# Optimization experiments

Hardware: AMD Instinct MI355X
Metric: run time of the kernel (lower is better)

The kernel has to match this reference:

```python
import jax, jax.numpy as jnp
import numpy as np

N_NODES = 100000
N_EDGES = 1600000
IN_CH = 128
HID = 64
OUT_CH = 10
N_GRAPHS = 64
NEG_SLOPE = 0.2   # GATv2Conv default negative_slope
EPS = 1e-16       # PyG softmax eps


def setup_inputs() -> dict:
    key = jax.random.key(0)
    ks = jax.random.split(key, 10)
    x = jax.random.normal(ks[0], (N_NODES, IN_CH), dtype=jnp.float32)
    edge_index = jax.random.randint(ks[1], (2, N_EDGES), 0, N_NODES, dtype=jnp.int64)
    batch = jnp.sort(jax.random.randint(ks[2], (N_NODES,), 0, N_GRAPHS, dtype=jnp.int64))
    s = 1.0 / np.sqrt(IN_CH)
    Wl = jax.random.uniform(ks[3], (IN_CH, HID), jnp.float32, -s, s)   # lin_l (source)
    Wr = jax.random.uniform(ks[4], (IN_CH, HID), jnp.float32, -s, s)   # lin_r (target)
    att = jax.random.uniform(ks[5], (HID,), jnp.float32, -1.0 / np.sqrt(HID), 1.0 / np.sqrt(HID))
    bias = jnp.zeros((HID,), jnp.float32)
    sf = 1.0 / np.sqrt(HID)
    fc_w = jax.random.uniform(ks[6], (HID, OUT_CH), jnp.float32, -sf, sf)
    fc_b = jax.random.uniform(ks[7], (OUT_CH,), jnp.float32, -sf, sf)
    return {"x": x, "Wl": Wl, "Wr": Wr, "att": att, "bias": bias,
            "fc_w": fc_w, "fc_b": fc_b, "edge_index": edge_index, "batch": batch}


def reference(x, Wl, Wr, att, bias, fc_w, fc_b, edge_index, batch):
    src, tgt = edge_index[0], edge_index[1]
    # GATv2Conv, heads=1: separate linear for source/target
    xl = x @ Wl                         # [N, H] messages (source side)
    xr = x @ Wr                         # [N, H] target side
    z = xl[src] + xr[tgt]               # [E, H]
    e = jnp.where(z > 0, z, NEG_SLOPE * z) @ att   # [E]
    # segment softmax over incoming edges of each target node
    m = jax.ops.segment_max(e, tgt, num_segments=N_NODES)      # [N]
    a = jnp.exp(e - m[tgt])                                    # [E]
    denom = jax.ops.segment_sum(a, tgt, num_segments=N_NODES)  # [N]
    alpha = a / (denom[tgt] + EPS)                             # [E]
    out = jax.ops.segment_sum(alpha[:, None] * xl[src], tgt, num_segments=N_NODES)
    out = out + bias                                           # [N, H]
    # global mean pool over graphs
    cnt = jax.ops.segment_sum(jnp.ones((N_NODES,), out.dtype), batch, num_segments=N_GRAPHS)
    pooled = jax.ops.segment_sum(out, batch, num_segments=N_GRAPHS) / jnp.maximum(cnt, 1.0)[:, None]
    h = jnp.where(pooled > 0, pooled, 0.01 * pooled)           # F.leaky_relu default slope
    # dropout is identity in eval / p=0
    return h @ fc_w + fc_b                                     # [G, OUT_CH]
```

## Files before the change

### kernel.cpp

```cpp
#include <hip/hip_runtime.h>
#include <hip/hip_bf16.h>

#define NN 100000
#define EE 1600000
#define CIN 128
#define HID 64
#define NG 64
#define NOUT 10
#define BSZ 32
#define NB 3125
#define CAP 768

__global__ __launch_bounds__(256) void k_gemm(
    const float* __restrict__ x, const float* __restrict__ Wl,
    const float* __restrict__ Wr, float* __restrict__ xl,
    float* __restrict__ xr) {
  __shared__ float Wlds[64 * 128];
  __shared__ float Xlds[64 * 68];
  const int tid = threadIdx.x;
  const int cg = tid & 31;
  const int ng = tid >> 5;
  const int ntiles = (NN + 63) >> 6;

  for (int tile = blockIdx.x; tile < ntiles; tile += gridDim.x) {
    const int nb = tile << 6;
    float acc[8][4];
#pragma unroll
    for (int i = 0; i < 8; ++i)
#pragma unroll
      for (int j = 0; j < 4; ++j) acc[i][j] = 0.f;

    for (int kc = 0; kc < CIN; kc += 64) {
      __syncthreads();
#pragma unroll
      for (int it = 0; it < 4; ++it) {
        int f = tid * 4 + it * 1024;
        int kk = f >> 6, c = f & 63;
        *(float4*)(Wlds + kk * 128 + c) =
            *(const float4*)(Wl + (kc + kk) * HID + c);
        *(float4*)(Wlds + kk * 128 + 64 + c) =
            *(const float4*)(Wr + (kc + kk) * HID + c);
      }
#pragma unroll
      for (int it = 0; it < 4; ++it) {
        int f = tid * 4 + it * 1024;
        int n = f >> 6, k = f & 63;
        int node = nb + n;
        float4 v;
        if (node < NN)
          v = *(const float4*)(x + (long)node * CIN + kc + k);
        else
          v = make_float4(0.f, 0.f, 0.f, 0.f);
        *(float4*)(Xlds + n * 68 + k) = v;
      }
      __syncthreads();

#pragma unroll 4
      for (int kk = 0; kk < 64; ++kk) {
        float4 w = *(const float4*)(Wlds + kk * 128 + cg * 4);
#pragma unroll
        for (int i = 0; i < 8; ++i) {
          float xv = Xlds[(ng * 8 + i) * 68 + kk];
          acc[i][0] = fmaf(xv, w.x, acc[i][0]);
          acc[i][1] = fmaf(xv, w.y, acc[i][1]);
          acc[i][2] = fmaf(xv, w.z, acc[i][2]);
          acc[i][3] = fmaf(xv, w.w, acc[i][3]);
        }
      }
    }
    const int cbase = cg * 4;
    float* dst = (cbase < 64) ? xl : xr;
    const int cb = cbase & 63;
#pragma unroll
    for (int i = 0; i < 8; ++i) {
      int node = nb + ng * 8 + i;
      if (node < NN) {
        float4 v = make_float4(acc[i][0], acc[i][1], acc[i][2], acc[i][3]);
        *(float4*)(dst + (long)node * HID + cb) = v;
      }
    }
  }
}

__global__ __launch_bounds__(256) void k_bucket(const int* __restrict__ ei,
                                                int* __restrict__ gcur,
                                                unsigned int* __restrict__ buckets) {
  __shared__ int hist[NB];
  __shared__ int lbase[NB];
  const int tid = threadIdx.x;
  const int base = blockIdx.x * 4096;
  for (int b = tid; b < NB; b += 256) hist[b] = 0;
  __syncthreads();
#pragma unroll
  for (int i = 0; i < 16; ++i) {
    int j = base + i * 256 + tid;
    if (j < EE) {
      int t = ei[EE + j];
      atomicAdd(&hist[t >> 5], 1);
    }
  }
  __syncthreads();
  for (int b = tid; b < NB; b += 256) {
    int c = hist[b];
    lbase[b] = (c > 0) ? atomicAdd(&gcur[b], c) : 0;
    hist[b] = 0;
  }
  __syncthreads();
#pragma unroll
  for (int i = 0; i < 16; ++i) {
    int j = base + i * 256 + tid;
    if (j < EE) {
      int s = ei[j];
      int t = ei[EE + j];
      int b2 = t >> 5;
      int lp = atomicAdd(&hist[b2], 1);
      int p = lbase[b2] + lp;
      if (p < CAP)
        buckets[(long)b2 * CAP + p] = ((unsigned)s << 5) | (unsigned)(t & 31);
    }
  }
}

__global__ __launch_bounds__(256) void k_pull2(
    const int* __restrict__ gcnt, const unsigned int* __restrict__ buckets,
    const float* __restrict__ xl, const float* __restrict__ xr,
    const float* __restrict__ att, const float* __restrict__ bias,
    const int* __restrict__ batch, float* __restrict__ pooled,
    float* __restrict__ cnt) {
  __shared__ unsigned int staged[CAP];
  __shared__ int lds_src[CAP];
  __shared__ int hist[BSZ];
  __shared__ int starts[BSZ + 1], cur[BSZ];
  __shared__ float pool2[2][HID];
  __shared__ float cnt2[2];
  const int tid = threadIdx.x;
  const int b = blockIdx.x;
  const int t0 = b << 5;
  const int ecnt = min(gcnt[b], CAP);

  if (tid < BSZ) hist[tid] = 0;
  if (tid < 2 * HID) ((float*)pool2)[tid] = 0.f;
  if (tid < 2) cnt2[tid] = 0.f;
  __syncthreads();

  for (int i = tid; i < ecnt; i += 256) {
    unsigned v = buckets[(long)b * CAP + i];
    staged[i] = v;
    atomicAdd(&hist[v & 31u], 1);
  }
  __syncthreads();

  if (tid < BSZ) {
    int v = hist[tid];
    int sum = v;
#pragma unroll
    for (int off = 1; off < BSZ; off <<= 1) {
      int t = __shfl_up(sum, off, 64);
      if (tid >= off) sum += t;
    }
    starts[tid] = sum - v;
    cur[tid] = sum - v;
    if (tid == BSZ - 1) starts[BSZ] = sum;
  }
  __syncthreads();

  for (int i = tid; i < ecnt; i += 256) {
    unsigned v = staged[i];
    int d = v & 31u;
    int p = atomicAdd(&cur[d], 1);
    lds_src[p] = (int)(v >> 5);
  }
  __syncthreads();

  const int g = tid & 15;
  const int grp = tid >> 4;
  const float4 a4 = *(const float4*)(att + g * 4);
  const float4 b4 = *(const float4*)(bias + g * 4);
  const int g0 = batch[t0];

#pragma unroll
  for (int rep = 0; rep < 2; ++rep) {
    const int d = grp * 2 + rep;
    const int n = t0 + d;
    const float4 xt = *(const float4*)(xr + (long)n * HID + g * 4);
    float4 acc = make_float4(0.f, 0.f, 0.f, 0.f);
    float den = 0.f;
    const int e0 = starts[d], e1 = starts[d + 1];
    int e = e0;
    for (; e + 1 < e1; e += 2) {
      const int s0 = lds_src[e];
      const int s1 = lds_src[e + 1];
      const float4 xs0 = *(const float4*)(xl + (long)s0 * HID + g * 4);
      const float4 xs1 = *(const float4*)(xl + (long)s1 * HID + g * 4);
      float zx0 = xs0.x + xt.x, zy0 = xs0.y + xt.y;
      float zz0 = xs0.z + xt.z, zw0 = xs0.w + xt.w;
      float zx1 = xs1.x + xt.x, zy1 = xs1.y + xt.y;
      float zz1 = xs1.z + xt.z, zw1 = xs1.w + xt.w;
      zx0 = zx0 > 0.f ? zx0 : 0.2f * zx0;
      zy0 = zy0 > 0.f ? zy0 : 0.2f * zy0;
      zz0 = zz0 > 0.f ? zz0 : 0.2f * zz0;
      zw0 = zw0 > 0.f ? zw0 : 0.2f * zw0;
      zx1 = zx1 > 0.f ? zx1 : 0.2f * zx1;
      zy1 = zy1 > 0.f ? zy1 : 0.2f * zy1;
      zz1 = zz1 > 0.f ? zz1 : 0.2f * zz1;
      zw1 = zw1 > 0.f ? zw1 : 0.2f * zw1;
      float p0 = zx0 * a4.x + zy0 * a4.y + zz0 * a4.z + zw0 * a4.w;
      float p1 = zx1 * a4.x + zy1 * a4.y + zz1 * a4.z + zw1 * a4.w;
      p0 += __shfl_xor(p0, 1, 16);
      p1 += __shfl_xor(p1, 1, 16);
      p0 += __shfl_xor(p0, 2, 16);
      p1 += __shfl_xor(p1, 2, 16);
      p0 += __shfl_xor(p0, 4, 16);
      p1 += __shfl_xor(p1, 4, 16);
      p0 += __shfl_xor(p0, 8, 16);
      p1 += __shfl_xor(p1, 8, 16);
      const float a0 = __expf(p0);
      const float a1 = __expf(p1);
      den += a0 + a1;
      acc.x = fmaf(a0, xs0.x, acc.x);
      acc.y = fmaf(a0, xs0.y, acc.y);
      acc.z = fmaf(a0, xs0.z, acc.z);
      acc.w = fmaf(a0, xs0.w, acc.w);
      acc.x = fmaf(a1, xs1.x, acc.x);
      acc.y = fmaf(a1, xs1.y, acc.y);
      acc.z = fmaf(a1, xs1.z, acc.z);
      acc.w = fmaf(a1, xs1.w, acc.w);
    }
    if (e < e1) {
      const int s0 = lds_src[e];
      const float4 xs0 = *(const float4*)(xl + (long)s0 * HID + g * 4);
      float zx0 = xs0.x + xt.x, zy0 = xs0.y + xt.y;
      float zz0 = xs0.z + xt.z, zw0 = xs0.w + xt.w;
      zx0 = zx0 > 0.f ? zx0 : 0.2f * zx0;
      zy0 = zy0 > 0.f ? zy0 : 0.2f * zy0;
      zz0 = zz0 > 0.f ? zz0 : 0.2f * zz0;
      zw0 = zw0 > 0.f ? zw0 : 0.2f * zw0;
      float p0 = zx0 * a4.x + zy0 * a4.y + zz0 * a4.z + zw0 * a4.w;
      p0 += __shfl_xor(p0, 1, 16);
      p0 += __shfl_xor(p0, 2, 16);
      p0 += __shfl_xor(p0, 4, 16);
      p0 += __shfl_xor(p0, 8, 16);
      const float a0 = __expf(p0);
      den += a0;
      acc.x = fmaf(a0, xs0.x, acc.x);
      acc.y = fmaf(a0, xs0.y, acc.y);
      acc.z = fmaf(a0, xs0.z, acc.z);
      acc.w = fmaf(a0, xs0.w, acc.w);
    }
    const float inv = 1.f / (den + 1e-16f);
    float4 v4 = make_float4(fmaf(acc.x, inv, b4.x), fmaf(acc.y, inv, b4.y),
                            fmaf(acc.z, inv, b4.z), fmaf(acc.w, inv, b4.w));
    const int gr = batch[n];
    const int idx = gr - g0;
    if (idx >= 0 && idx < 2) {
      atomicAdd(&pool2[idx][g * 4 + 0], v4.x);
      atomicAdd(&pool2[idx][g * 4 + 1], v4.y);
      atomicAdd(&pool2[idx][g * 4 + 2], v4.z);
      atomicAdd(&pool2[idx][g * 4 + 3], v4.w);
      if (g == 0) atomicAdd(&cnt2[idx], 1.f);
    } else {
      atomicAdd(pooled + gr * HID + g * 4 + 0, v4.x);
      atomicAdd(pooled + gr * HID + g * 4 + 1, v4.y);
      atomicAdd(pooled + gr * HID + g * 4 + 2, v4.z);
      atomicAdd(pooled + gr * HID + g * 4 + 3, v4.w);
      if (g == 0) atomicAdd(cnt + gr, 1.f);
    }
  }
  __syncthreads();
  if (tid < 2 * HID) {
    const int which = tid >> 6, c = tid & 63;
    const int gg = g0 + which;
    const float val = pool2[which][c];
    if (gg < NG && val != 0.f) atomicAdd(pooled + gg * HID + c, val);
  }
  if (tid < 2) {
    const int gg = g0 + tid;
    if (gg < NG && cnt2[tid] != 0.f) atomicAdd(cnt + gg, cnt2[tid]);
  }
}

__global__ void k_final(const float* __restrict__ pooled,
                        const float* __restrict__ cnt,
                        const float* __restrict__ fc_w,
                        const float* __restrict__ fc_b,
                        float* __restrict__ out) {
  const int tid = threadIdx.x;
  if (tid >= NG * NOUT) return;
  const int gr = tid / NOUT, o = tid % NOUT;
  const float cg = fmaxf(cnt[gr], 1.0f);
  float acc = fc_b[o];
#pragma unroll 8
  for (int h = 0; h < HID; ++h) {
    float pv = pooled[gr * HID + h] / cg;
    float hv = pv > 0.f ? pv : 0.01f * pv;
    acc = fmaf(hv, fc_w[h * NOUT + o], acc);
  }
  out[gr * NOUT + o] = acc;
}

extern "C" void kernel_launch(void* const* d_in, const int* in_sizes, int n_in,
                              void* d_out, int out_size, void* d_ws,
                              size_t ws_size, hipStream_t stream) {
  const float* x = (const float*)d_in[0];
  const float* Wl = (const float*)d_in[1];
  const float* Wr = (const float*)d_in[2];
  const float* att = (const float*)d_in[3];
  const float* bias = (const float*)d_in[4];
  const float* fc_w = (const float*)d_in[5];
  const float* fc_b = (const float*)d_in[6];
  const int* ei = (const int*)d_in[7];
  const int* batch = (const int*)d_in[8];
  float* out = (float*)d_out;

  float* ws = (float*)d_ws;
  float* xl = ws;
  float* xr = xl + (long)NN * HID;
  unsigned int* buckets = (unsigned int*)(xr + (long)NN * HID);
  int* gcur = (int*)(buckets + (long)NB * CAP);
  float* pooled = (float*)(gcur + NB);
  float* cnt = pooled + NG * HID;

  hipMemsetAsync(gcur, 0, (size_t)(NB + NG * HID + NG) * sizeof(int), stream);

  k_gemm<<<768, 256, 0, stream>>>(x, Wl, Wr, xl, xr);
  k_bucket<<<(EE + 4095) / 4096, 256, 0, stream>>>(ei, gcur, buckets);
  k_pull2<<<NB, 256, 0, stream>>>(gcur, buckets, xl, xr, att, bias, batch,
                                  pooled, cnt);
  k_final<<<1, NG * NOUT, 0, stream>>>(pooled, cnt, fc_w, fc_b, out);
}
```

Before: 284.1 us.

## Use bf16 MFMA GEMM, store xl/xr as bf16, simplify edge bucketing

The projection GEMM now runs on bf16 MFMA instructions, using swizzled LDS tiles and a small kernel that pre-transposes and converts the weights. Its outputs xl/xr are stored as bf16, which halves the bytes of every random gather in the edge-pull kernel. The bucketing kernel drops its per-block LDS histogram and instead does one global atomic per edge. The bf16 rounding of x, W and the projections adds numerical error, and the per-edge global atomics may contend more than the old two-pass scheme.

Result: slower. 354.5 us (+24.8%).

```diff
diff --git a/kernel.cpp b/kernel.cpp
--- a/kernel.cpp
+++ b/kernel.cpp
@@ -11,119 +11,138 @@
 #define NB 3125
 #define CAP 768
 
+typedef short s16x8 __attribute__((ext_vector_type(8)));
+typedef float f32x4 __attribute__((ext_vector_type(4)));
+
+__device__ __forceinline__ unsigned short f2b(float f) {
+  unsigned int b = __float_as_uint(f);
+  return (unsigned short)((b + 0x7FFFu + ((b >> 16) & 1u)) >> 16);
+}
+__device__ __forceinline__ float b2f(unsigned short h) {
+  return __uint_as_float(((unsigned int)h) << 16);
+}
+
+__global__ __launch_bounds__(256) void k_prep(const float* __restrict__ Wl,
+                                              const float* __restrict__ Wr,
+                                              unsigned short* __restrict__ Wt) {
+  int flat = blockIdx.x * 2048 + threadIdx.x;
+  for (int i = 0; i < 8; ++i, flat += 256) {
+    int n = flat & 127, k = flat >> 7;
+    float v = (n < 64) ? Wl[k * 64 + n] : Wr[k * 64 + (n - 64)];
+    Wt[n * 128 + k] = f2b(v);
+  }
+}
+
 __global__ __launch_bounds__(256) void k_gemm(
-    const float* __restrict__ x, const float* __restrict__ Wl,
-    const float* __restrict__ Wr, float* __restrict__ xl,
-    float* __restrict__ xr) {
-  __shared__ float Wlds[64 * 128];
-  __shared__ float Xlds[64 * 68];
+    const float* __restrict__ x, const unsigned short* __restrict__ Wt,
+    unsigned short* __restrict__ xl, unsigned short* __restrict__ xr) {
+  __shared__ unsigned short A[128 * 128];
+  __shared__ unsigned short B[128 * 128];
   const int tid = threadIdx.x;
-  const int cg = tid & 31;
-  const int ng = tid >> 5;
-  const int ntiles = (NN + 63) >> 6;
-
-  for (int tile = blockIdx.x; tile < ntiles; tile += gridDim.x) {
-    const int nb = tile << 6;
-    float acc[8][4];
-#pragma unroll
-    for (int i = 0; i < 8; ++i)
-#pragma unroll
-      for (int j = 0; j < 4; ++j) acc[i][j] = 0.f;
-
-    for (int kc = 0; kc < CIN; kc += 64) {
-      __syncthreads();
-#pragma unroll
-      for (int it = 0; it < 4; ++it) {
-        int f = tid * 4 + it * 1024;
-        int kk = f >> 6, c = f & 63;
-        *(float4*)(Wlds + kk * 128 + c) =
-            *(const float4*)(Wl + (kc + kk) * HID + c);
-        *(float4*)(Wlds + kk * 128 + 64 + c) =
-            *(const float4*)(Wr + (kc + kk) * HID + c);
+  const int lane = tid & 63;
+  const int w = tid >> 6;
+  const int nb = blockIdx.x * 128;
+
+  {
+    int u = tid;
+#pragma unroll
+    for (int i = 0; i < 8; ++i, u += 256) {
+      int n = u >> 4, slot = u & 15;
+      uint4 v = *(const uint4*)((const char*)Wt + u * 16);
+      int addr = n * 256 + ((slot * 16) ^ ((n & 7) << 4));
+      *(uint4*)((char*)B + addr) = v;
+    }
+  }
+  {
+    int f = tid;
+#pragma unroll
+    for (int i = 0; i < 16; ++i, f += 256) {
+      int row = f >> 5, c4 = f & 31;
+      int node = nb + row;
+      float4 v = make_float4(0.f, 0.f, 0.f, 0.f);
+      if (node < NN) v = *(const float4*)(x + (long)node * CIN + c4 * 4);
+      uint2 p;
+      p.x = (unsigned)f2b(v.x) | ((unsigned)f2b(v.y) << 16);
+      p.y = (unsigned)f2b(v.z) | ((unsigned)f2b(v.w) << 16);
+      int base16 = row * 256 + (((c4 >> 1) << 4) ^ ((row & 7) << 4));
+      *(uint2*)((char*)A + base16 + (c4 & 1) * 8) = p;
+    }
+  }
+  __syncthreads();
+
+  const int m0 = w * 32;
+  f32x4 acc[2][8];
+#pragma unroll
+  for (int mt = 0; mt < 2; ++mt)
+#pragma unroll
+    for (int nt = 0; nt < 8; ++nt) acc[mt][nt] = (f32x4){0.f, 0.f, 0.f, 0.f};
+
+#pragma unroll
+  for (int ks = 0; ks < 4; ++ks) {
+    const int kb2 = (ks * 32 + (lane >> 4) * 8) * 2;
+    const int r0 = m0 + (lane & 15);
+    const int r1 = r0 + 16;
+    s16x8 a0 = *(const s16x8*)((char*)A + r0 * 256 + (kb2 ^ ((r0 & 7) << 4)));
+    s16x8 a1 = *(const s16x8*)((char*)A + r1 * 256 + (kb2 ^ ((r1 & 7) << 4)));
+#pragma unroll
+    for (int nt = 0; nt < 8; ++nt) {
+      const int col = nt * 16 + (lane & 15);
+      s16x8 b =
+          *(const s16x8*)((char*)B + col * 256 + (kb2 ^ ((col & 7) << 4)));
+      acc[0][nt] =
+          __builtin_amdgcn_mfma_f32_16x16x32_bf16(a0, b, acc[0][nt], 0, 0, 0);
+      acc[1][nt] =
+          __builtin_amdgcn_mfma_f32_16x16x32_bf16(a1, b, acc[1][nt], 0, 0, 0);
+    }
+  }
+  __syncthreads();
+
+#pragma unroll
+  for (int mt = 0; mt < 2; ++mt) {
+    const int rowb = m0 + mt * 16 + (lane >> 4) * 4;
+#pragma unroll
+    for (int nt = 0; nt < 8; ++nt) {
+      const int col = nt * 16 + (lane & 15);
+#pragma unroll
+      for (int r = 0; r < 4; ++r)
+        *((unsigned short*)A + (rowb + r) * 128 + col) = f2b(acc[mt][nt][r]);
+    }
+  }
+  __syncthreads();
+
+  {
+    int u = tid;
+#pragma unroll
+    for (int i = 0; i < 8; ++i, u += 256) {
+      int row = u >> 4, slot = u & 15;
+      int node = nb + row;
+      if (node < NN) {
+        uint4 v = *(const uint4*)((const char*)A + row * 256 + slot * 16);
+        if (slot < 8)
+          *(uint4*)((char*)xl + (long)node * 128 + slot * 16) = v;
+        else
+          *(uint4*)((char*)xr + (long)node * 128 + (slot - 8) * 16) = v;
       }
-#pragma unroll
-      for (int it = 0; it < 4; ++it) {
-        int f = tid * 4 + it * 1024;
-        int n = f >> 6, k = f & 63;
-        int node = nb + n;
-        float4 v;
-        if (node < NN)
-          v = *(const float4*)(x + (long)node * CIN + kc + k);
-        else
-          v = make_float4(0.f, 0.f, 0.f, 0.f);
-        *(float4*)(Xlds + n * 68 + k) = v;
-      }
-      __syncthreads();
-
-#pragma unroll 4
-      for (int kk = 0; kk < 64; ++kk) {
-        float4 w = *(const float4*)(Wlds + kk * 128 + cg * 4);
-#pragma unroll
-        for (int i = 0; i < 8; ++i) {
-          float xv = Xlds[(ng * 8 + i) * 68 + kk];
-          acc[i][0] = fmaf(xv, w.x, acc[i][0]);
-          acc[i][1] = fmaf(xv, w.y, acc[i][1]);
-          acc[i][2] = fmaf(xv, w.z, acc[i][2]);
-          acc[i][3] = fmaf(xv, w.w, acc[i][3]);
-        }
-      }
-    }
-    const int cbase = cg * 4;
-    float* dst = (cbase < 64) ? xl : xr;
-    const int cb = cbase & 63;
-#pragma unroll
-    for (int i = 0; i < 8; ++i) {
-      int node = nb + ng * 8 + i;
-      if (node < NN) {
-        float4 v = make_float4(acc[i][0], acc[i][1], acc[i][2], acc[i][3]);
-        *(float4*)(dst + (long)node * HID + cb) = v;
-      }
-    }
-  }
-}
-
-__global__ __launch_bounds__(256) void k_bucket(const int* __restrict__ ei,
-                                                int* __restrict__ gcur,
-                                                unsigned int* __restrict__ buckets) {
-  __shared__ int hist[NB];
-  __shared__ int lbase[NB];
-  const int tid = threadIdx.x;
-  const int base = blockIdx.x * 4096;
-  for (int b = tid; b < NB; b += 256) hist[b] = 0;
-  __syncthreads();
-#pragma unroll
-  for (int i = 0; i < 16; ++i) {
-    int j = base + i * 256 + tid;
-    if (j < EE) {
-      int t = ei[EE + j];
-      atomicAdd(&hist[t >> 5], 1);
-    }
-  }
-  __syncthreads();
-  for (int b = tid; b < NB; b += 256) {
-    int c = hist[b];
-    lbase[b] = (c > 0) ? atomicAdd(&gcur[b], c) : 0;
-    hist[b] = 0;
-  }
-  __syncthreads();
-#pragma unroll
-  for (int i = 0; i < 16; ++i) {
-    int j = base + i * 256 + tid;
-    if (j < EE) {
-      int s = ei[j];
-      int t = ei[EE + j];
-      int b2 = t >> 5;
-      int lp = atomicAdd(&hist[b2], 1);
-      int p = lbase[b2] + lp;
-      if (p < CAP)
-        buckets[(long)b2 * CAP + p] = ((unsigned)s << 5) | (unsigned)(t & 31);
-    }
-  }
+    }
+  }
+}
+
+__global__ __launch_bounds__(256) void k_bucket(
+    const int* __restrict__ ei, int* __restrict__ gcur,
+    unsigned int* __restrict__ buckets) {
+  const int j = blockIdx.x * 256 + threadIdx.x;
+  if (j >= EE) return;
+  const int s = ei[j];
+  const int t = ei[EE + j];
+  const int b = t >> 5;
+  const int p = atomicAdd(gcur + b, 1);
+  if (p < CAP)
+    buckets[(long)b * CAP + p] = ((unsigned)s << 5) | (unsigned)(t & 31);
 }
 
 __global__ __launch_bounds__(256) void k_pull2(
     const int* __restrict__ gcnt, const unsigned int* __restrict__ buckets,
-    const float* __restrict__ xl, const float* __restrict__ xr,
+    const unsigned short* __restrict__ xl, const unsigned short* __restrict__ xr,
     const float* __restrict__ att, const float* __restrict__ bias,
     const int* __restrict__ batch, float* __restrict__ pooled,
     float* __restrict__ cnt) {
@@ -182,7 +201,9 @@
   for (int rep = 0; rep < 2; ++rep) {
     const int d = grp * 2 + rep;
     const int n = t0 + d;
-    const float4 xt = *(const float4*)(xr + (long)n * HID + g * 4);
+    const ushort4 ut = *(const ushort4*)(xr + (long)n * HID + g * 4);
+    const float xtx = b2f(ut.x), xty = b2f(ut.y);
+    const float xtz = b2f(ut.z), xtw = b2f(ut.w);
     float4 acc = make_float4(0.f, 0.f, 0.f, 0.f);
     float den = 0.f;
     const int e0 = starts[d], e1 = starts[d + 1];
@@ -190,12 +211,14 @@
     for (; e + 1 < e1; e += 2) {
       const int s0 = lds_src[e];
       const int s1 = lds_src[e + 1];
-      const float4 xs0 = *(const float4*)(xl + (long)s0 * HID + g * 4);
-      const float4 xs1 = *(const float4*)(xl + (long)s1 * HID + g * 4);
-      float zx0 = xs0.x + xt.x, zy0 = xs0.y + xt.y;
-      float zz0 = xs0.z + xt.z, zw0 = xs0.w + xt.w;
-      float zx1 = xs1.x + xt.x, zy1 = xs1.y + xt.y;
-      float zz1 = xs1.z + xt.z, zw1 = xs1.w + xt.w;
+      const ushort4 u0 = *(const ushort4*)(xl + (long)s0 * HID + g * 4);
+      const ushort4 u1 = *(const ushort4*)(xl + (long)s1 * HID + g * 4);
+      const float x0x = b2f(u0.x), x0y = b2f(u0.y);
+      const float x0z = b2f(u0.z), x0w = b2f(u0.w);
+      const float x1x = b2f(u1.x), x1y = b2f(u1.y);
+      const float x1z = b2f(u1.z), x1w = b2f(u1.w);
+      float zx0 = x0x + xtx, zy0 = x0y + xty, zz0 = x0z + xtz, zw0 = x0w + xtw;
+      float zx1 = x1x + xtx, zy1 = x1y + xty, zz1 = x1z + xtz, zw1 = x1w + xtw;
       zx0 = zx0 > 0.f ? zx0 : 0.2f * zx0;
       zy0 = zy0 > 0.f ? zy0 : 0.2f * zy0;
       zz0 = zz0 > 0.f ? zz0 : 0.2f * zz0;
@@ -217,20 +240,21 @@
       const float a0 = __expf(p0);
       const float a1 = __expf(p1);
       den += a0 + a1;
-      acc.x = fmaf(a0, xs0.x, acc.x);
-      acc.y = fmaf(a0, xs0.y, acc.y);
-      acc.z = fmaf(a0, xs0.z, acc.z);
-      acc.w = fmaf(a0, xs0.w, acc.w);
-      acc.x = fmaf(a1, xs1.x, acc.x);
-      acc.y = fmaf(a1, xs1.y, acc.y);
-      acc.z = fmaf(a1, xs1.z, acc.z);
-      acc.w = fmaf(a1, xs1.w, acc.w);
+      acc.x = fmaf(a0, x0x, acc.x);
+      acc.y = fmaf(a0, x0y, acc.y);
+      acc.z = fmaf(a0, x0z, acc.z);
+      acc.w = fmaf(a0, x0w, acc.w);
+      acc.x = fmaf(a1, x1x, acc.x);
+      acc.y = fmaf(a1, x1y, acc.y);
+      acc.z = fmaf(a1, x1z, acc.z);
+      acc.w = fmaf(a1, x1w, acc.w);
     }
     if (e < e1) {
       const int s0 = lds_src[e];
-      const float4 xs0 = *(const float4*)(xl + (long)s0 * HID + g * 4);
-      float zx0 = xs0.x + xt.x, zy0 = xs0.y + xt.y;
-      float zz0 = xs0.z + xt.z, zw0 = xs0.w + xt.w;
+      const ushort4 u0 = *(const ushort4*)(xl + (long)s0 * HID + g * 4);
+      const float x0x = b2f(u0.x), x0y = b2f(u0.y);
+      const float x0z = b2f(u0.z), x0w = b2f(u0.w);
+      float zx0 = x0x + xtx, zy0 = x0y + xty, zz0 = x0z + xtz, zw0 = x0w + xtw;
       zx0 = zx0 > 0.f ? zx0 : 0.2f * zx0;
       zy0 = zy0 > 0.f ? zy0 : 0.2f * zy0;
       zz0 = zz0 > 0.f ? zz0 : 0.2f * zz0;
@@ -242,10 +266,10 @@
       p0 += __shfl_xor(p0, 8, 16);
       const float a0 = __expf(p0);
       den += a0;
-      acc.x = fmaf(a0, xs0.x, acc.x);
-      acc.y = fmaf(a0, xs0.y, acc.y);
-      acc.z = fmaf(a0, xs0.z, acc.z);
-      acc.w = fmaf(a0, xs0.w, acc.w);
+      acc.x = fmaf(a0, x0x, acc.x);
+      acc.y = fmaf(a0, x0y, acc.y);
+      acc.z = fmaf(a0, x0z, acc.z);
+      acc.w = fmaf(a0, x0w, acc.w);
     }
     const float inv = 1.f / (den + 1e-16f);
     float4 v4 = make_float4(fmaf(acc.x, inv, b4.x), fmaf(acc.y, inv, b4.y),
@@ -312,18 +336,19 @@
   const int* batch = (const int*)d_in[8];
   float* out = (float*)d_out;
 
-  float* ws = (float*)d_ws;
-  float* xl = ws;
-  float* xr = xl + (long)NN * HID;
-  unsigned int* buckets = (unsigned int*)(xr + (long)NN * HID);
+  unsigned short* xl = (unsigned short*)d_ws;
+  unsigned short* xr = xl + (long)NN * HID;
+  unsigned short* Wt = xr + (long)NN * HID;
+  unsigned int* buckets = (unsigned int*)(Wt + 128 * 128);
   int* gcur = (int*)(buckets + (long)NB * CAP);
   float* pooled = (float*)(gcur + NB);
   float* cnt = pooled + NG * HID;
 
   hipMemsetAsync(gcur, 0, (size_t)(NB + NG * HID + NG) * sizeof(int), stream);
 
-  k_gemm<<<768, 256, 0, stream>>>(x, Wl, Wr, xl, xr);
-  k_bucket<<<(EE + 4095) / 4096, 256, 0, stream>>>(ei, gcur, buckets);
+  k_prep<<<8, 256, 0, stream>>>(Wl, Wr, Wt);
+  k_gemm<<<(NN + 127) / 128, 256, 0, stream>>>(x, Wt, xl, xr);
+  k_bucket<<<(EE + 255) / 256, 256, 0, stream>>>(ei, gcur, buckets);
   k_pull2<<<NB, 256, 0, stream>>>(gcur, buckets, xl, xr, att, bias, batch,
                                   pooled, cnt);
   k_final<<<1, NG * NOUT, 0, stream>>>(pooled, cnt, fc_w, fc_b, out);
```
